# Performance work log

Measured on AMD Instinct MI355X. Metric: run time of the kernel, lower is better.

## Reference

```python
import jax, jax.numpy as jnp
import numpy as np

N, H, F = 131072, 256, 4096
MIN_FRAG = 3
LN_EPS = 1e-5
NORM_EPS = 1e-12
CONSISTENCY_FACTOR = 0.03
INTERMOLECULAR_WEIGHT = 0.2
SCALING_FACTOR = 0.05  # initial_strength at epoch 0 (progressive schedule, eval mode)


def _normalize(x):
    # torch F.normalize(p=2, dim=1): x / max(||x||, eps)
    n = jnp.linalg.norm(x, axis=-1, keepdims=True)
    return x / jnp.maximum(n, NORM_EPS)


def _frag_consistency(feat, frag_ids, valid):
    # size-weighted sum of per-fragment mean deviations == mean deviation over valid atoms
    m = valid.astype(feat.dtype)[:, None]
    seg_sum = jax.ops.segment_sum(feat * m, frag_ids, num_segments=F)
    seg_cnt = jax.ops.segment_sum(m, frag_ids, num_segments=F)
    means = seg_sum / jnp.maximum(seg_cnt, 1.0)  # scatter-mean over valid atoms
    sim = jnp.sum(_normalize(feat) * _normalize(means)[frag_ids], axis=-1)  # [N]
    dev = (1.0 - sim) * valid.astype(feat.dtype)
    return jnp.sum(dev) / jnp.maximum(jnp.sum(valid.astype(feat.dtype)), 1.0)


def setup_inputs() -> dict:
    key = jax.random.key(0)
    ks = jax.random.split(key, 8)
    return {
        "scalar_short": jax.random.normal(ks[0], (N, H), jnp.float32),
        "scalar_long": jax.random.normal(ks[1], (N, H), jnp.float32),
        "vector_short": jax.random.normal(ks[2], (N, 3, H), jnp.float32),
        "vector_long": jax.random.normal(ks[3], (N, 3, H), jnp.float32),
        "fragment_ids": jax.random.randint(ks[4], (N,), 0, F, dtype=jnp.int32),
        "ln_gamma": jnp.ones((H,), jnp.float32),
        "ln_beta": jnp.zeros((H,), jnp.float32),
        "W1": jax.random.normal(ks[5], (H, H), jnp.float32) / np.sqrt(H),
        "b1": jnp.zeros((H,), jnp.float32),
        "Wv": jax.random.normal(ks[6], (H, H), jnp.float32) / np.sqrt(H),
    }


def reference(scalar_short, scalar_long, vector_short, vector_long, fragment_ids,
              ln_gamma, ln_beta, W1, b1, Wv):
    # valid_mask: atoms belonging to fragments of size >= MIN_FRAG
    sizes = jax.ops.segment_sum(jnp.ones((N,), jnp.float32), fragment_ids, num_segments=F)
    valid = sizes[fragment_ids] >= MIN_FRAG  # [N] bool

    # scalar_projector: LayerNorm -> Linear -> SiLU (dropout identity at eval)
    mu = jnp.mean(scalar_short, axis=-1, keepdims=True)
    var = jnp.var(scalar_short, axis=-1, keepdims=True)
    xh = (scalar_short - mu) / jnp.sqrt(var + LN_EPS) * ln_gamma + ln_beta
    scalar_features = jax.nn.silu(xh @ W1.T + b1)  # [N, H]

    intra = _frag_consistency(scalar_features, fragment_ids, valid)

    # vector branch: per-atom magnitude = mean over 3 spatial comps of ||.||_2 over hidden
    vec_mag = jnp.mean(jnp.linalg.norm(vector_short, axis=2), axis=1, keepdims=True)  # [N,1]
    # Linear(bias=False) on mag.expand(-1,H) then [:, :1] == silu(mag * sum(Wv[0,:]))
    w0 = jnp.sum(Wv[0])
    vector_features = jax.nn.silu(vec_mag * w0)  # [N,1]
    vec_loss = _frag_consistency(vector_features, fragment_ids, valid)

    # interfragment differentiation over ALL atoms (no valid mask)
    cnt = jax.ops.segment_sum(jnp.ones((N, 1), jnp.float32), fragment_ids, num_segments=F)
    sfrag = jax.ops.segment_sum(scalar_features, fragment_ids, num_segments=F) / jnp.maximum(cnt, 1.0)
    vfrag = jax.ops.segment_sum(vec_mag, fragment_ids, num_segments=F) / jnp.maximum(cnt, 1.0)
    combined = _normalize(jnp.concatenate([sfrag, vfrag], axis=1))  # [F, H+1]
    sim = combined @ combined.T  # [F, F]
    off_sum = jnp.sum(sim) - jnp.trace(sim)
    inter = off_sum / (F * F - F + 1e-6)

    total = intra + vec_loss + INTERMOLECULAR_WEIGHT * inter
    return CONSISTENCY_FACTOR * total * SCALING_FACTOR
```

## Files before the change

### kernel.cpp

```cpp
#include <hip/hip_runtime.h>
#include <hip/hip_bf16.h>
#include <stdint.h>

#define NA 131072
#define HD 256
#define NF 4096
#define MINFRAG 3
#define LN_EPS 1e-5f
#define NEPS 1e-12f

#define OFF_CNT    0ull
#define OFF_VSUM   16384ull
#define OFF_VFSUM  32768ull
#define OFF_NVSUM  49152ull
#define OFF_FILL   65536ull
#define OFF_DBL    81920ull
#define OFF_SSUM   86016ull
#define OFF_NSUM   4280320ull
#define ZERO_BYTES 8474624ull
#define OFF_OFFS   8474624ull
#define OFF_SVEC   8491008ull
#define OFF_C0     8492032ull
#define OFF_W0     8493056ull
#define OFF_GBF    8493568ull
#define OFF_ORDER  8624640ull
#define OFF_PART   9150464ull

#define IDX_TRACE 257
#define IDX_DEVS  258
#define IDX_DEVV  259
#define IDX_VCNT  260
#define FRAGB 256
#define PSTRIDE 264

typedef __attribute__((ext_vector_type(8))) short short8;
typedef __attribute__((ext_vector_type(4))) float f32x4;
union F4S8 { float4 f; short8 s; };
union BFU { __hip_bfloat16 b; unsigned short u; };

__device__ __forceinline__ unsigned short f2b(float x) {
    BFU t; t.b = __float2bfloat16(x); return t.u;
}
__device__ __forceinline__ float b2f(unsigned short u) {
    return __uint_as_float(((uint32_t)u) << 16);
}
__device__ __forceinline__ float silu_f(float x) {
    return x * __builtin_amdgcn_rcpf(1.f + __expf(-x));
}

__global__ __launch_bounds__(256) void k_prep(
    const float* __restrict__ W1, const float* __restrict__ gamma,
    const float* __restrict__ beta, const float* __restrict__ b1,
    const float* __restrict__ Wv,
    unsigned short* __restrict__ Gbf, float* __restrict__ svec,
    float* __restrict__ c0, float* __restrict__ w0, float4* __restrict__ z) {
    __shared__ float red[8];
    int o = blockIdx.x;
    int t = threadIdx.x;
    {
        float4 zv = {0.f, 0.f, 0.f, 0.f};
        z[o * 256 + t] = zv;
    }
    if (o < HD) {
        float w = W1[(size_t)o * HD + t];
        unsigned short gb = f2b(w * gamma[t]);
        Gbf[(size_t)o * HD + t] = gb;
        float sp = b2f(gb);
        float cp = w * beta[t];
#pragma unroll
        for (int m = 32; m; m >>= 1) { sp += __shfl_xor(sp, m, 64); cp += __shfl_xor(cp, m, 64); }
        int wv = t >> 6;
        if ((t & 63) == 0) { red[wv] = sp; red[4 + wv] = cp; }
        __syncthreads();
        if (t == 0) {
            svec[o] = red[0] + red[1] + red[2] + red[3];
            c0[o]   = red[4] + red[5] + red[6] + red[7] + b1[o];
        }
    } else if (o == HD) {
        float v = Wv[t];
#pragma unroll
        for (int m = 32; m; m >>= 1) v += __shfl_xor(v, m, 64);
        int wv = t >> 6;
        if ((t & 63) == 0) red[wv] = v;
        __syncthreads();
        if (t == 0) w0[0] = red[0] + red[1] + red[2] + red[3];
    }
}

__global__ __launch_bounds__(256) void k_stats(
    const float* __restrict__ vs, const int* __restrict__ fid,
    const float* __restrict__ w0p,
    int* __restrict__ cnt, float* __restrict__ vsum,
    float* __restrict__ vfsum, float* __restrict__ nvsum) {
    int gwave = (blockIdx.x * blockDim.x + threadIdx.x) >> 6;
    int lane = threadIdx.x & 63;
    int nw = (gridDim.x * blockDim.x) >> 6;
    int g = lane >> 4, sl = lane & 15;
    float w0 = w0p[0];
    for (int i0 = gwave * 4; i0 < NA; i0 += nw * 4) {
        int i = i0 + g;
        const float* vb = vs + (size_t)i * 3 * HD;
        float q0 = 0.f, q1 = 0.f, q2 = 0.f;
#pragma unroll
        for (int j = 0; j < 4; ++j) {
            float4 a = ((const float4*)(vb))[j * 16 + sl];
            float4 b = ((const float4*)(vb + HD))[j * 16 + sl];
            float4 c = ((const float4*)(vb + 2 * HD))[j * 16 + sl];
            q0 += a.x * a.x + a.y * a.y + a.z * a.z + a.w * a.w;
            q1 += b.x * b.x + b.y * b.y + b.z * b.z + b.w * b.w;
            q2 += c.x * c.x + c.y * c.y + c.z * c.z + c.w * c.w;
        }
#pragma unroll
        for (int m = 1; m < 16; m <<= 1) {
            q0 += __shfl_xor(q0, m, 64);
            q1 += __shfl_xor(q1, m, 64);
            q2 += __shfl_xor(q2, m, 64);
        }
        if (sl == 0) {
            float vm = (sqrtf(q0) + sqrtf(q1) + sqrtf(q2)) * (1.f / 3.f);
            float vf = silu_f(vm * w0);
            float nv = vf / fmaxf(fabsf(vf), NEPS);
            int f = fid[i];
            atomicAdd(&cnt[f], 1);
            atomicAdd(&vsum[f], vm);
            atomicAdd(&vfsum[f], vf);
            atomicAdd(&nvsum[f], nv);
        }
    }
}

__global__ __launch_bounds__(256) void k_scan(const int* __restrict__ cnt,
                                              int* __restrict__ offs) {
    __shared__ int wsum[4];
    int t = threadIdx.x;
    int base = t * 16;
    int c[16];
    int tot = 0;
#pragma unroll
    for (int j = 0; j < 16; ++j) { c[j] = cnt[base + j]; tot += c[j]; }
    int lane = t & 63, w = t >> 6;
    int v = tot;
#pragma unroll
    for (int d = 1; d < 64; d <<= 1) {
        int o = __shfl_up(v, d, 64);
        if (lane >= d) v += o;
    }
    if (lane == 63) wsum[w] = v;
    __syncthreads();
    int wbase = 0;
    for (int i = 0; i < w; ++i) wbase += wsum[i];
    int run = wbase + v - tot;
#pragma unroll
    for (int j = 0; j < 16; ++j) { offs[base + j] = run; run += c[j]; }
}

__global__ __launch_bounds__(256) void k_scatter(
    const int* __restrict__ fid, const int* __restrict__ offs,
    int* __restrict__ fill, int* __restrict__ order) {
    int i = blockIdx.x * blockDim.x + threadIdx.x;
    if (i < NA) {
        int f = fid[i];
        int p = atomicAdd(&fill[f], 1);
        order[offs[f] + p] = i;
    }
}

__global__ __launch_bounds__(256) void k_gemm(
    const float* __restrict__ A, const unsigned short* __restrict__ Gbf,
    const float* __restrict__ svec, const float* __restrict__ c0,
    const int* __restrict__ order, const int* __restrict__ fid,
    const int* __restrict__ offs, const int* __restrict__ cnt,
    float* __restrict__ ssum, float* __restrict__ nsum) {
    __shared__ float4 As16[64 * 32];
    __shared__ float muS[64], rsS[64], rnS[64];
    __shared__ float sqL[64][4];
    __shared__ int ridS[64], fragS[64];

    int tid = threadIdx.x;
    int lane = tid & 63, wid = tid >> 6;
    int r0 = blockIdx.x * 64;

    if (tid < 64) {
        int gi = order[r0 + tid];
        ridS[tid] = gi;
        fragS[tid] = fid[gi];
    }
    __syncthreads();

    {
        const float4* A4 = (const float4*)A;
        int kcL = lane >> 4, c4L = lane & 15;
#pragma unroll
        for (int jb = 0; jb < 2; ++jb) {
            float4 v[8];
#pragma unroll
            for (int j = 0; j < 8; ++j) {
                int row = wid * 16 + jb * 8 + j;
                v[j] = A4[(size_t)ridS[row] * 64 + lane];
            }
#pragma unroll
            for (int j = 0; j < 8; ++j) {
                int row = wid * 16 + jb * 8 + j;
                float s1 = v[j].x + v[j].y + v[j].z + v[j].w;
                float s2 = v[j].x * v[j].x + v[j].y * v[j].y +
                           v[j].z * v[j].z + v[j].w * v[j].w;
#pragma unroll
                for (int m = 32; m; m >>= 1) {
                    s1 += __shfl_xor(s1, m, 64);
                    s2 += __shfl_xor(s2, m, 64);
                }
                if (lane == 0) {
                    float mu_ = s1 * (1.f / HD);
                    float var = s2 * (1.f / HD) - mu_ * mu_;
                    muS[row] = mu_;
                    rsS[row] = rsqrtf(var + LN_EPS);
                }
                ushort4 pk;
                pk.x = f2b(v[j].x); pk.y = f2b(v[j].y);
                pk.z = f2b(v[j].z); pk.w = f2b(v[j].w);
                int slot = row * 32 + kcL * 8 + ((c4L >> 1) ^ (row & 7));
                ((ushort4*)&As16[slot])[c4L & 1] = pk;
            }
        }
    }
    __syncthreads();

    int lg = lane >> 4;
    const unsigned short* bp[4];
#pragma unroll
    for (int ni = 0; ni < 4; ++ni)
        bp[ni] = Gbf + (size_t)(wid * 64 + ni * 16 + (lane & 15)) * HD + lg * 8;

    f32x4 acc[4][4] = {};
#pragma unroll
    for (int kc = 0; kc < 4; ++kc) {
        short8 bfr[2][4];
#pragma unroll
        for (int kk = 0; kk < 2; ++kk)
#pragma unroll
            for (int ni = 0; ni < 4; ++ni)
                bfr[kk][ni] = *(const short8*)(bp[ni] + kc * 64 + kk * 32);
#pragma unroll
        for (int kk = 0; kk < 2; ++kk) {
            int jp = kk * 4 + lg;
            short8 a[4];
#pragma unroll
            for (int mi = 0; mi < 4; ++mi) {
                int r = mi * 16 + (lane & 15);
                F4S8 t_; t_.f = As16[r * 32 + kc * 8 + (jp ^ (r & 7))];
                a[mi] = t_.s;
            }
#pragma unroll
            for (int mi = 0; mi < 4; ++mi)
#pragma unroll
                for (int ni = 0; ni < 4; ++ni)
                    acc[mi][ni] = __builtin_amdgcn_mfma_f32_16x16x32_bf16(
                        a[mi], bfr[kk][ni], acc[mi][ni], 0, 0, 0);
        }
    }
    __syncthreads();

    float sv[4], cv[4];
#pragma unroll
    for (int ni = 0; ni < 4; ++ni) {
        int c = wid * 64 + ni * 16 + (lane & 15);
        sv[ni] = svec[c];
        cv[ni] = c0[c];
    }
    unsigned short* featS = (unsigned short*)As16;
    float sq[4][4];
#pragma unroll
    for (int mi = 0; mi < 4; ++mi)
#pragma unroll
        for (int q = 0; q < 4; ++q) {
            int rl = mi * 16 + (lane >> 4) * 4 + q;
            float mu_ = muS[rl], rs_ = rsS[rl];
            float sqa = 0.f;
#pragma unroll
            for (int ni = 0; ni < 4; ++ni) {
                int c = wid * 64 + ni * 16 + (lane & 15);
                float pre = rs_ * (acc[mi][ni][q] - mu_ * sv[ni]) + cv[ni];
                unsigned short us = f2b(silu_f(pre));
                featS[rl * 256 + (c ^ ((rl & 7) << 2))] = us;
                float fr = b2f(us);
                sqa += fr * fr;
            }
            sq[mi][q] = sqa;
        }
#pragma unroll
    for (int mi = 0; mi < 4; ++mi)
#pragma unroll
        for (int q = 0; q < 4; ++q) {
            float s_ = sq[mi][q];
            s_ += __shfl_xor(s_, 1, 64);
            s_ += __shfl_xor(s_, 2, 64);
            s_ += __shfl_xor(s_, 4, 64);
            s_ += __shfl_xor(s_, 8, 64);
            if ((lane & 15) == 0) sqL[mi * 16 + (lane >> 4) * 4 + q][wid] = s_;
        }
    __syncthreads();
    if (tid < 64) {
        float t = sqL[tid][0] + sqL[tid][1] + sqL[tid][2] + sqL[tid][3];
        rnS[tid] = 1.f / fmaxf(sqrtf(t), NEPS);
    }
    __syncthreads();
    int cc = wid * 64 + lane;
    float sAcc = 0.f, nAcc = 0.f;
    int curF = fragS[0];
    for (int row = 0; row < 64; ++row) {
        int f = fragS[row];
        if (f != curF) {
            int gs = offs[curF], n = cnt[curF];
            if (gs >= r0 && gs + n <= r0 + 64) {
                ssum[(size_t)curF * HD + cc] = sAcc;
                nsum[(size_t)curF * HD + cc] = nAcc;
            } else {
                atomicAdd(&ssum[(size_t)curF * HD + cc], sAcc);
                atomicAdd(&nsum[(size_t)curF * HD + cc], nAcc);
            }
            sAcc = 0.f; nAcc = 0.f; curF = f;
        }
        float v = b2f(featS[row * 256 + (cc ^ ((row & 7) << 2))]);
        sAcc += v;
        nAcc = fmaf(v, rnS[row], nAcc);
    }
    {
        int gs = offs[curF], n = cnt[curF];
        if (gs >= r0 && gs + n <= r0 + 64) {
            ssum[(size_t)curF * HD + cc] = sAcc;
            nsum[(size_t)curF * HD + cc] = nAcc;
        } else {
            atomicAdd(&ssum[(size_t)curF * HD + cc], sAcc);
            atomicAdd(&nsum[(size_t)curF * HD + cc], nAcc);
        }
    }
}

__global__ __launch_bounds__(256) void k_frag(
    const float* __restrict__ ssum, const float* __restrict__ nsum,
    const int* __restrict__ cnt, const float* __restrict__ vsum,
    const float* __restrict__ vfsum, const float* __restrict__ nvsum,
    double* __restrict__ partial) {
    __shared__ double lred[4][PSTRIDE];
    int tid = threadIdx.x;
    int lane = tid & 63, wid = tid >> 6;
    int gwave = blockIdx.x * 4 + wid;
    const int nw = FRAGB * 4;

    double la0 = 0, la1 = 0, la2 = 0, la3 = 0;
    double lv = 0, ltr = 0, lvc = 0, ldS = 0, ldV = 0;

    for (int f = gwave; f < NF; f += nw) {
        float4 s = ((const float4*)(ssum + (size_t)f * HD))[lane];
        float4 nn = ((const float4*)(nsum + (size_t)f * HD))[lane];
        int c = cnt[f];
        float ssq = s.x * s.x + s.y * s.y + s.z * s.z + s.w * s.w;
        float dsn = nn.x * s.x + nn.y * s.y + nn.z * s.z + nn.w * s.w;
#pragma unroll
        for (int m = 32; m; m >>= 1) {
            ssq += __shfl_xor(ssq, m, 64);
            dsn += __shfl_xor(dsn, m, 64);
        }
        float inv_all = 1.f / fmaxf((float)c, 1.f);
        float m0 = s.x * inv_all, m1 = s.y * inv_all, m2 = s.z * inv_all, m3 = s.w * inv_all;
        float ssq_mean = ssq * inv_all * inv_all;
        float vfr = vsum[f] * inv_all;
        float nrm2 = ssq_mean + vfr * vfr;
        float inv = 1.f / fmaxf(sqrtf(nrm2), NEPS);
        la0 += (double)(m0 * inv);
        la1 += (double)(m1 * inv);
        la2 += (double)(m2 * inv);
        la3 += (double)(m3 * inv);
        if (lane == 0) {
            lv += (double)(vfr * inv);
            ltr += (double)(nrm2 * inv * inv);
            if (c >= MINFRAG) {
                lvc += (double)c;
                float denom = fmaxf(sqrtf(ssq), NEPS);
                ldS += (double)c - (double)(dsn / denom);
                float vfm = vfsum[f] * inv_all;
                float vsgn = vfm / fmaxf(fabsf(vfm), NEPS);
                ldV += (double)c - (double)(vsgn * nvsum[f]);
            }
        }
    }
    lred[wid][4 * lane + 0] = la0;
    lred[wid][4 * lane + 1] = la1;
    lred[wid][4 * lane + 2] = la2;
    lred[wid][4 * lane + 3] = la3;
    if (lane == 0) {
        lred[wid][256] = lv;
        lred[wid][IDX_TRACE] = ltr;
        lred[wid][IDX_DEVS] = ldS;
        lred[wid][IDX_DEVV] = ldV;
        lred[wid][IDX_VCNT] = lvc;
    }
    __syncthreads();
    for (int idx = tid; idx < 261; idx += 256)
        partial[(size_t)blockIdx.x * PSTRIDE + idx] =
            lred[0][idx] + lred[1][idx] + lred[2][idx] + lred[3][idx];
}

__global__ __launch_bounds__(256) void k_final(const double* __restrict__ partial,
                                               float* __restrict__ out) {
    __shared__ double fin[PSTRIDE];
    int t = threadIdx.x;
    for (int idx = t; idx < 261; idx += 256) {
        double s = 0;
        for (int b = 0; b < FRAGB; ++b) s += partial[(size_t)b * PSTRIDE + idx];
        fin[idx] = s;
    }
    __syncthreads();
    if (t == 0) {
        double s2 = 0;
        for (int d = 0; d < 257; ++d) s2 += fin[d] * fin[d];
        double off = s2 - fin[IDX_TRACE];
        double inter = off / ((double)NF * NF - NF + 1e-6);
        double vc = fmax(fin[IDX_VCNT], 1.0);
        double total = fin[IDX_DEVS] / vc + fin[IDX_DEVV] / vc + 0.2 * inter;
        out[0] = (float)(0.03 * 0.05 * total);
    }
}

extern "C" void kernel_launch(void* const* d_in, const int* in_sizes, int n_in,
                              void* d_out, int out_size, void* d_ws, size_t ws_size,
                              hipStream_t stream) {
    const float* scalar_short = (const float*)d_in[0];
    const float* vector_short = (const float*)d_in[2];
    const int* fragment_ids = (const int*)d_in[4];
    const float* ln_gamma = (const float*)d_in[5];
    const float* ln_beta = (const float*)d_in[6];
    const float* W1 = (const float*)d_in[7];
    const float* b1 = (const float*)d_in[8];
    const float* Wv = (const float*)d_in[9];
    float* out = (float*)d_out;

    char* ws = (char*)d_ws;
    int* cnt = (int*)(ws + OFF_CNT);
    float* vsum = (float*)(ws + OFF_VSUM);
    float* vfsum = (float*)(ws + OFF_VFSUM);
    float* nvsum = (float*)(ws + OFF_NVSUM);
    int* fill = (int*)(ws + OFF_FILL);
    float* ssum = (float*)(ws + OFF_SSUM);
    float* nsum = (float*)(ws + OFF_NSUM);
    int* offs = (int*)(ws + OFF_OFFS);
    float* svec = (float*)(ws + OFF_SVEC);
    float* c0 = (float*)(ws + OFF_C0);
    float* w0 = (float*)(ws + OFF_W0);
    unsigned short* Gbf = (unsigned short*)(ws + OFF_GBF);
    int* order = (int*)(ws + OFF_ORDER);
    double* partial = (double*)(ws + OFF_PART);

    k_prep<<<2069, 256, 0, stream>>>(W1, ln_gamma, ln_beta, b1, Wv, Gbf, svec,
                                     c0, w0, (float4*)ws);
    k_stats<<<8192, 256, 0, stream>>>(vector_short, fragment_ids, w0, cnt, vsum, vfsum, nvsum);
    k_scan<<<1, 256, 0, stream>>>(cnt, offs);
    k_scatter<<<NA / 256, 256, 0, stream>>>(fragment_ids, offs, fill, order);
    k_gemm<<<NA / 64, 256, 0, stream>>>(scalar_short, Gbf, svec, c0, order,
                                        fragment_ids, offs, cnt, ssum, nsum);
    k_frag<<<FRAGB, 256, 0, stream>>>(ssum, nsum, cnt, vsum, vfsum, nvsum, partial);
    k_final<<<1, 256, 0, stream>>>(partial, out);
}
```

Measured before the change: 214.3 us.

## Fuse vector-magnitude stats into GEMM kernel via interleaved block roles

The vector_short pass that computed per-atom magnitudes and fragment atomics is moved out of its own kernel. Odd blocks of the GEMM launch now handle it, and the fragment count histogram becomes a small separate kernel. The goal is to overlap the bandwidth-heavy vector read with the compute-heavy GEMM blocks and get the large stats pass off the critical path before the sort. The cost is an extra tiny histogram kernel, plus mixed block roles that may hurt occupancy balance and L2 behaviour.

```diff
diff --git a/kernel.cpp b/kernel.cpp
--- a/kernel.cpp
+++ b/kernel.cpp
@@ -87,46 +87,10 @@
     }
 }
 
-__global__ __launch_bounds__(256) void k_stats(
-    const float* __restrict__ vs, const int* __restrict__ fid,
-    const float* __restrict__ w0p,
-    int* __restrict__ cnt, float* __restrict__ vsum,
-    float* __restrict__ vfsum, float* __restrict__ nvsum) {
-    int gwave = (blockIdx.x * blockDim.x + threadIdx.x) >> 6;
-    int lane = threadIdx.x & 63;
-    int nw = (gridDim.x * blockDim.x) >> 6;
-    int g = lane >> 4, sl = lane & 15;
-    float w0 = w0p[0];
-    for (int i0 = gwave * 4; i0 < NA; i0 += nw * 4) {
-        int i = i0 + g;
-        const float* vb = vs + (size_t)i * 3 * HD;
-        float q0 = 0.f, q1 = 0.f, q2 = 0.f;
-#pragma unroll
-        for (int j = 0; j < 4; ++j) {
-            float4 a = ((const float4*)(vb))[j * 16 + sl];
-            float4 b = ((const float4*)(vb + HD))[j * 16 + sl];
-            float4 c = ((const float4*)(vb + 2 * HD))[j * 16 + sl];
-            q0 += a.x * a.x + a.y * a.y + a.z * a.z + a.w * a.w;
-            q1 += b.x * b.x + b.y * b.y + b.z * b.z + b.w * b.w;
-            q2 += c.x * c.x + c.y * c.y + c.z * c.z + c.w * c.w;
-        }
-#pragma unroll
-        for (int m = 1; m < 16; m <<= 1) {
-            q0 += __shfl_xor(q0, m, 64);
-            q1 += __shfl_xor(q1, m, 64);
-            q2 += __shfl_xor(q2, m, 64);
-        }
-        if (sl == 0) {
-            float vm = (sqrtf(q0) + sqrtf(q1) + sqrtf(q2)) * (1.f / 3.f);
-            float vf = silu_f(vm * w0);
-            float nv = vf / fmaxf(fabsf(vf), NEPS);
-            int f = fid[i];
-            atomicAdd(&cnt[f], 1);
-            atomicAdd(&vsum[f], vm);
-            atomicAdd(&vfsum[f], vf);
-            atomicAdd(&nvsum[f], nv);
-        }
-    }
+__global__ __launch_bounds__(256) void k_hist(
+    const int* __restrict__ fid, int* __restrict__ cnt) {
+    int i = blockIdx.x * 256 + threadIdx.x;
+    if (i < NA) atomicAdd(&cnt[fid[i]], 1);
 }
 
 __global__ __launch_bounds__(256) void k_scan(const int* __restrict__ cnt,
@@ -165,11 +129,14 @@
     }
 }
 
-__global__ __launch_bounds__(256) void k_gemm(
+__global__ __launch_bounds__(256) void k_merged(
     const float* __restrict__ A, const unsigned short* __restrict__ Gbf,
     const float* __restrict__ svec, const float* __restrict__ c0,
+    const float* __restrict__ vs, const float* __restrict__ w0p,
     const int* __restrict__ order, const int* __restrict__ fid,
     const int* __restrict__ offs, const int* __restrict__ cnt,
+    float* __restrict__ vsum, float* __restrict__ vfsum,
+    float* __restrict__ nvsum,
     float* __restrict__ ssum, float* __restrict__ nsum) {
     __shared__ float4 As16[64 * 32];
     __shared__ float muS[64], rsS[64], rnS[64];
@@ -178,7 +145,46 @@
 
     int tid = threadIdx.x;
     int lane = tid & 63, wid = tid >> 6;
-    int r0 = blockIdx.x * 64;
+    int b = blockIdx.x;
+
+    if (b & 1) {
+        int g = lane >> 4, sl = lane & 15;
+        float w0 = w0p[0];
+        int base = (b >> 1) * 64 + wid * 16;
+#pragma unroll 1
+        for (int it = 0; it < 4; ++it) {
+            int i = base + it * 4 + g;
+            const float* vb = vs + (size_t)i * 3 * HD;
+            float q0 = 0.f, q1 = 0.f, q2 = 0.f;
+#pragma unroll
+            for (int j = 0; j < 4; ++j) {
+                float4 a = ((const float4*)(vb))[j * 16 + sl];
+                float4 bb = ((const float4*)(vb + HD))[j * 16 + sl];
+                float4 c = ((const float4*)(vb + 2 * HD))[j * 16 + sl];
+                q0 += a.x * a.x + a.y * a.y + a.z * a.z + a.w * a.w;
+                q1 += bb.x * bb.x + bb.y * bb.y + bb.z * bb.z + bb.w * bb.w;
+                q2 += c.x * c.x + c.y * c.y + c.z * c.z + c.w * c.w;
+            }
+#pragma unroll
+            for (int m = 1; m < 16; m <<= 1) {
+                q0 += __shfl_xor(q0, m, 64);
+                q1 += __shfl_xor(q1, m, 64);
+                q2 += __shfl_xor(q2, m, 64);
+            }
+            if (sl == 0) {
+                float vm = (sqrtf(q0) + sqrtf(q1) + sqrtf(q2)) * (1.f / 3.f);
+                float vf = silu_f(vm * w0);
+                float nv = vf / fmaxf(fabsf(vf), NEPS);
+                int f = fid[i];
+                atomicAdd(&vsum[f], vm);
+                atomicAdd(&vfsum[f], vf);
+                atomicAdd(&nvsum[f], nv);
+            }
+        }
+        return;
+    }
+
+    int r0 = (b >> 1) * 64;
 
     if (tid < 64) {
         int gi = order[r0 + tid];
@@ -453,11 +459,12 @@
 
     k_prep<<<2069, 256, 0, stream>>>(W1, ln_gamma, ln_beta, b1, Wv, Gbf, svec,
                                      c0, w0, (float4*)ws);
-    k_stats<<<8192, 256, 0, stream>>>(vector_short, fragment_ids, w0, cnt, vsum, vfsum, nvsum);
+    k_hist<<<NA / 256, 256, 0, stream>>>(fragment_ids, cnt);
     k_scan<<<1, 256, 0, stream>>>(cnt, offs);
     k_scatter<<<NA / 256, 256, 0, stream>>>(fragment_ids, offs, fill, order);
-    k_gemm<<<NA / 64, 256, 0, stream>>>(scalar_short, Gbf, svec, c0, order,
-                                        fragment_ids, offs, cnt, ssum, nsum);
+    k_merged<<<4096, 256, 0, stream>>>(scalar_short, Gbf, svec, c0,
+                                       vector_short, w0, order, fragment_ids,
+                                       offs, cnt, vsum, vfsum, nvsum, ssum, nsum);
     k_frag<<<FRAGB, 256, 0, stream>>>(ssum, nsum, cnt, vsum, vfsum, nvsum, partial);
     k_final<<<1, 256, 0, stream>>>(partial, out);
 }
```

Measured after the change: 227.8 us. 6.3% more time.
